# Performance work log

Measured on AMD Instinct MI355X. Metric: run time of the kernel, lower is better.

The kernel has to match this reference:

```python
import jax, jax.numpy as jnp
import numpy as np

# FreqEncoder constants (from init_kwargs)
X_DIM = 3
MIN_DEG = 0.0
MAX_DEG = 8.0
NUM_SCALES = 8            # max_deg - min_deg
RES = 128                 # 2 ** log2_res
NUM_CH = 8                # num_feats (channels per grid)
STD = 0.001
P = 262144                # number of sample points


def setup_inputs() -> dict:
    key = jax.random.key(0)
    k1, k2 = jax.random.split(key)
    x = jax.random.uniform(k1, (P, X_DIM), dtype=jnp.float32)
    # learned 1D grids: [num_scales*2*x_dim, num_channels, res]
    features = jax.random.normal(k2, (NUM_SCALES * 2 * X_DIM, NUM_CH, RES), dtype=jnp.float32) * STD
    return {"x": x, "features": features}


def reference(x, features):
    S, D, C, res = NUM_SCALES, X_DIM, NUM_CH, RES
    N = S * 2 * D  # number of 1D grids
    p = x.shape[0]

    # scales = 2 ** linspace(min_deg, max_deg, num_scales)  (matches torch.linspace)
    scales = 2.0 ** jnp.linspace(MIN_DEG, MAX_DEG, S).astype(x.dtype)  # [S]

    xb = x[:, None, :] * scales[None, :, None]                     # [P, S, D]
    latent = jnp.sin(jnp.stack([xb, xb + 0.5 * jnp.pi], axis=-2))  # [P, S, 2, D]

    # values in [-1, 1] used as grid_sample y-coords; one grid per (s, phase, d)
    v = latent.reshape(p, N).T                                     # [N, P]

    # align_corners=True bilinear unnormalization along the res axis
    pos = (v + 1.0) * 0.5 * (res - 1)                              # [N, P] in [0, res-1]
    i0f = jnp.floor(pos)
    frac = pos - i0f                                               # [N, P]
    i0 = jnp.clip(i0f, 0, res - 1).astype(jnp.int32)
    i1 = jnp.clip(i0 + 1, 0, res - 1)

    idx0 = jnp.broadcast_to(i0[:, None, :], (N, C, p))
    idx1 = jnp.broadcast_to(i1[:, None, :], (N, C, p))
    f0 = jnp.take_along_axis(features, idx0, axis=2)               # [N, C, P]
    f1 = jnp.take_along_axis(features, idx1, axis=2)               # [N, C, P]
    fs = f0 * (1.0 - frac[:, None, :]) + f1 * frac[:, None, :]     # [N, C, P]

    # [N, C, P] -> [S, 2, D, C, P] -> [P, C, S, 2, D], add residual, flatten
    fs = fs.reshape(S, 2, D, C, p).transpose(4, 3, 0, 1, 2)
    out = (fs + latent[:, None, :, :, :]).reshape(p, C * S * 2 * D)

    # use_identity=True: prepend raw coordinates
    return jnp.concatenate([x, out], axis=-1)                      # [P, 3 + 384]
```

## Files before the change

kernel.cpp:

```cpp
#include <hip/hip_runtime.h>
#include <hip/hip_bf16.h>
#include <stdint.h>


constexpr int P_PTS = 262144;
constexpr int S_SC  = 8;
constexpr int D_DIM = 3;
constexpr int C_CH  = 8;
constexpr int RES   = 128;
constexpr int N_GR  = S_SC * 2 * D_DIM;
constexpr int OW    = 3 + C_CH * N_GR;
constexpr int KPB   = 32;
constexpr int CHUNKS = 8;
constexpr int PPB   = KPB * CHUNKS;
constexpr int BLK   = 1024;

constexpr float ENC_SCALE = 256.0f;
constexpr float DEC_SCALE = 1.0f / 256.0f;
constexpr float INV_2PI   = 0.15915494309189535f;

constexpr int LDS_TABLE_B = N_GR * RES * 8;
constexpr int LDS_SOUT_B  = KPB * OW * 4;
constexpr int LDS_SX_B    = PPB * D_DIM * 4;
constexpr int LDS_TOTAL_B = LDS_TABLE_B + 2 * LDS_SOUT_B + LDS_SX_B;

typedef float f32x2 __attribute__((ext_vector_type(2)));

__device__ uint2 g_tap[N_GR * RES];

__global__ __launch_bounds__(256) void feat_pack_kernel(const float* __restrict__ f) {
    int t = blockIdx.x * 256 + threadIdx.x;
    if (t >= N_GR * RES) return;
    int n = t / RES, i = t % RES;

    uint32_t d0, d1;
    {
        float a = f[(n * C_CH + 0) * RES + i] * ENC_SCALE;
        float b = f[(n * C_CH + 1) * RES + i] * ENC_SCALE;
        float c = f[(n * C_CH + 2) * RES + i] * ENC_SCALE;
        float e = f[(n * C_CH + 3) * RES + i] * ENC_SCALE;
        int lo = __builtin_amdgcn_cvt_pk_fp8_f32(a, b, 0, false);
        d0 = (uint32_t)__builtin_amdgcn_cvt_pk_fp8_f32(c, e, lo, true);
    }
    {
        float a = f[(n * C_CH + 4) * RES + i] * ENC_SCALE;
        float b = f[(n * C_CH + 5) * RES + i] * ENC_SCALE;
        float c = f[(n * C_CH + 6) * RES + i] * ENC_SCALE;
        float e = f[(n * C_CH + 7) * RES + i] * ENC_SCALE;
        int lo = __builtin_amdgcn_cvt_pk_fp8_f32(a, b, 0, false);
        d1 = (uint32_t)__builtin_amdgcn_cvt_pk_fp8_f32(c, e, lo, true);
    }
    g_tap[t] = make_uint2(d0, d1);
}

__global__ __launch_bounds__(1024) void freq_encode_kernel(const float* __restrict__ x,
                                                           float* __restrict__ out) {
    extern __shared__ char smem[];
    uint2* ld_tap = reinterpret_cast<uint2*>(smem);
    float* s_out0 = reinterpret_cast<float*>(smem + LDS_TABLE_B);
    float* s_out1 = reinterpret_cast<float*>(smem + LDS_TABLE_B + LDS_SOUT_B);
    float* s_x    = reinterpret_cast<float*>(smem + LDS_TABLE_B + 2 * LDS_SOUT_B);

    const int tid   = threadIdx.x;
    const int pbase = blockIdx.x * PPB;

    for (int i = tid; i < N_GR * RES; i += BLK) ld_tap[i] = g_tap[i];
    for (int i = tid; i < PPB * D_DIM; i += BLK) s_x[i] = x[(size_t)pbase * D_DIM + i];
    __syncthreads();

    auto do_compute = [&](int p0l, float* sbuf) {
        if (tid < KPB * D_DIM) {
            sbuf[(tid / D_DIM) * OW + (tid % D_DIM)] = s_x[p0l * D_DIM + tid];
        }
        for (int u = tid; u < KPB * N_GR; u += BLK) {
            int pl = u / N_GR;
            int n  = u % N_GR;
            int s  = n / (2 * D_DIM);
            int r  = n % (2 * D_DIM);
            int ph = r / D_DIM;
            int d  = r % D_DIM;

            float xv    = s_x[(p0l + pl) * D_DIM + d];
            float scale = exp2f((float)s * (8.0f / 7.0f));
            float rv    = fmaf(xv * scale, INV_2PI, ph ? 0.25f : 0.0f);
            float lat   = __builtin_amdgcn_sinf(__builtin_amdgcn_fractf(rv));

            float pos  = (lat + 1.0f) * 63.5f;
            float i0f  = floorf(pos);
            float frac = pos - i0f;
            int   i0   = (int)i0f;
            i0 = max(0, min(i0, RES - 1));
            int   i1   = min(i0 + 1, RES - 1);

            uint2 t0 = ld_tap[n * RES + i0];
            uint2 t1 = ld_tap[n * RES + i1];

            f32x2 a01 = __builtin_amdgcn_cvt_pk_f32_fp8(t0.x, false);
            f32x2 a23 = __builtin_amdgcn_cvt_pk_f32_fp8(t0.x, true);
            f32x2 a45 = __builtin_amdgcn_cvt_pk_f32_fp8(t0.y, false);
            f32x2 a67 = __builtin_amdgcn_cvt_pk_f32_fp8(t0.y, true);
            f32x2 b01 = __builtin_amdgcn_cvt_pk_f32_fp8(t1.x, false);
            f32x2 b23 = __builtin_amdgcn_cvt_pk_f32_fp8(t1.x, true);
            f32x2 b45 = __builtin_amdgcn_cvt_pk_f32_fp8(t1.y, false);
            f32x2 b67 = __builtin_amdgcn_cvt_pk_f32_fp8(t1.y, true);

            float omd = (1.0f - frac) * DEC_SCALE;
            float frd = frac * DEC_SCALE;

            float* dst = &sbuf[pl * OW + 3 + n];
            dst[0 * N_GR] = fmaf(a01[0], omd, fmaf(b01[0], frd, lat));
            dst[1 * N_GR] = fmaf(a01[1], omd, fmaf(b01[1], frd, lat));
            dst[2 * N_GR] = fmaf(a23[0], omd, fmaf(b23[0], frd, lat));
            dst[3 * N_GR] = fmaf(a23[1], omd, fmaf(b23[1], frd, lat));
            dst[4 * N_GR] = fmaf(a45[0], omd, fmaf(b45[0], frd, lat));
            dst[5 * N_GR] = fmaf(a45[1], omd, fmaf(b45[1], frd, lat));
            dst[6 * N_GR] = fmaf(a67[0], omd, fmaf(b67[0], frd, lat));
            dst[7 * N_GR] = fmaf(a67[1], omd, fmaf(b67[1], frd, lat));
        }
    };

    auto do_store = [&](int p0l, const float* sbuf) {
        constexpr int NV = KPB * OW / 4;
        const float4* src = reinterpret_cast<const float4*>(sbuf);
        float4*       dst = reinterpret_cast<float4*>(out + ((size_t)pbase + p0l) * OW);
        for (int i = tid; i < NV; i += BLK) {
            dst[i] = src[i];
        }
    };

    do_compute(0, s_out0);
    __syncthreads();
    for (int ch = 1; ch < CHUNKS; ++ch) {
        float* cur  = (ch & 1) ? s_out1 : s_out0;
        float* prev = (ch & 1) ? s_out0 : s_out1;
        do_store((ch - 1) * KPB, prev);
        do_compute(ch * KPB, cur);
        __syncthreads();
    }
    do_store((CHUNKS - 1) * KPB, ((CHUNKS - 1) & 1) ? s_out1 : s_out0);
}

extern "C" void kernel_launch(void* const* d_in, const int* in_sizes, int n_in,
                              void* d_out, int out_size, void* d_ws, size_t ws_size,
                              hipStream_t stream) {
    const float* x    = (const float*)d_in[0];
    const float* feat = (const float*)d_in[1];
    float*       out  = (float*)d_out;

    int n_taps = N_GR * RES;
    feat_pack_kernel<<<(n_taps + 255) / 256, 256, 0, stream>>>(feat);

    freq_encode_kernel<<<P_PTS / PPB, BLK, LDS_TOTAL_B, stream>>>(x, out);
}
```

Baseline: 88.80 us.

## Replace double-buffered chunk pipeline with single buffer and nontemporal stores

Halves the points per chunk and doubles the chunk count, so each chunk's 768 work items fit in one pass of the 1024-thread block. The double-buffered compute/store overlap is replaced by a single staging buffer with two barriers per chunk. Output writes now use nontemporal stores. This cuts LDS use, which may allow more resident blocks, and tightens launch bounds, but it serialises compute and store within each block and adds barriers.

New measurement: 101.4 us. 1.14x slower.

```diff
diff --git a/kernel.cpp b/kernel.cpp
--- a/kernel.cpp
+++ b/kernel.cpp
@@ -10,8 +10,8 @@
 constexpr int RES   = 128;
 constexpr int N_GR  = S_SC * 2 * D_DIM;
 constexpr int OW    = 3 + C_CH * N_GR;
-constexpr int KPB   = 32;
-constexpr int CHUNKS = 8;
+constexpr int KPB   = 16;
+constexpr int CHUNKS = 16;
 constexpr int PPB   = KPB * CHUNKS;
 constexpr int BLK   = 1024;
 
@@ -22,9 +22,10 @@
 constexpr int LDS_TABLE_B = N_GR * RES * 8;
 constexpr int LDS_SOUT_B  = KPB * OW * 4;
 constexpr int LDS_SX_B    = PPB * D_DIM * 4;
-constexpr int LDS_TOTAL_B = LDS_TABLE_B + 2 * LDS_SOUT_B + LDS_SX_B;
+constexpr int LDS_TOTAL_B = LDS_TABLE_B + LDS_SOUT_B + LDS_SX_B;
 
 typedef float f32x2 __attribute__((ext_vector_type(2)));
+typedef float f32x4 __attribute__((ext_vector_type(4)));
 
 __device__ uint2 g_tap[N_GR * RES];
 
@@ -53,28 +54,30 @@
     g_tap[t] = make_uint2(d0, d1);
 }
 
-__global__ __launch_bounds__(1024) void freq_encode_kernel(const float* __restrict__ x,
-                                                           float* __restrict__ out) {
+__global__ __launch_bounds__(1024, 8) void freq_encode_kernel(const float* __restrict__ x,
+                                                              float* __restrict__ out) {
     extern __shared__ char smem[];
     uint2* ld_tap = reinterpret_cast<uint2*>(smem);
-    float* s_out0 = reinterpret_cast<float*>(smem + LDS_TABLE_B);
-    float* s_out1 = reinterpret_cast<float*>(smem + LDS_TABLE_B + LDS_SOUT_B);
-    float* s_x    = reinterpret_cast<float*>(smem + LDS_TABLE_B + 2 * LDS_SOUT_B);
+    float* s_out  = reinterpret_cast<float*>(smem + LDS_TABLE_B);
+    float* s_x    = reinterpret_cast<float*>(smem + LDS_TABLE_B + LDS_SOUT_B);
 
     const int tid   = threadIdx.x;
     const int pbase = blockIdx.x * PPB;
 
     for (int i = tid; i < N_GR * RES; i += BLK) ld_tap[i] = g_tap[i];
-    for (int i = tid; i < PPB * D_DIM; i += BLK) s_x[i] = x[(size_t)pbase * D_DIM + i];
+    if (tid < PPB * D_DIM) s_x[tid] = x[(size_t)pbase * D_DIM + tid];
     __syncthreads();
 
-    auto do_compute = [&](int p0l, float* sbuf) {
+    for (int ch = 0; ch < CHUNKS; ++ch) {
+        const int p0l = ch * KPB;
+
         if (tid < KPB * D_DIM) {
-            sbuf[(tid / D_DIM) * OW + (tid % D_DIM)] = s_x[p0l * D_DIM + tid];
+            s_out[(tid / D_DIM) * OW + (tid % D_DIM)] = s_x[p0l * D_DIM + tid];
         }
-        for (int u = tid; u < KPB * N_GR; u += BLK) {
-            int pl = u / N_GR;
-            int n  = u % N_GR;
+
+        if (tid < KPB * N_GR) {
+            int pl = tid / N_GR;
+            int n  = tid % N_GR;
             int s  = n / (2 * D_DIM);
             int r  = n % (2 * D_DIM);
             int ph = r / D_DIM;
@@ -107,7 +110,7 @@
             float omd = (1.0f - frac) * DEC_SCALE;
             float frd = frac * DEC_SCALE;
 
-            float* dst = &sbuf[pl * OW + 3 + n];
+            float* dst = &s_out[pl * OW + 3 + n];
             dst[0 * N_GR] = fmaf(a01[0], omd, fmaf(b01[0], frd, lat));
             dst[1 * N_GR] = fmaf(a01[1], omd, fmaf(b01[1], frd, lat));
             dst[2 * N_GR] = fmaf(a23[0], omd, fmaf(b23[0], frd, lat));
@@ -117,27 +120,16 @@
             dst[6 * N_GR] = fmaf(a67[0], omd, fmaf(b67[0], frd, lat));
             dst[7 * N_GR] = fmaf(a67[1], omd, fmaf(b67[1], frd, lat));
         }
-    };
+        __syncthreads();
 
-    auto do_store = [&](int p0l, const float* sbuf) {
         constexpr int NV = KPB * OW / 4;
-        const float4* src = reinterpret_cast<const float4*>(sbuf);
-        float4*       dst = reinterpret_cast<float4*>(out + ((size_t)pbase + p0l) * OW);
+        const f32x4* src = reinterpret_cast<const f32x4*>(s_out);
+        f32x4*       dst = reinterpret_cast<f32x4*>(out + ((size_t)pbase + p0l) * OW);
         for (int i = tid; i < NV; i += BLK) {
-            dst[i] = src[i];
+            __builtin_nontemporal_store(src[i], &dst[i]);
         }
-    };
-
-    do_compute(0, s_out0);
-    __syncthreads();
-    for (int ch = 1; ch < CHUNKS; ++ch) {
-        float* cur  = (ch & 1) ? s_out1 : s_out0;
-        float* prev = (ch & 1) ? s_out0 : s_out1;
-        do_store((ch - 1) * KPB, prev);
-        do_compute(ch * KPB, cur);
         __syncthreads();
     }
-    do_store((CHUNKS - 1) * KPB, ((CHUNKS - 1) & 1) ? s_out1 : s_out0);
 }
 
 extern "C" void kernel_launch(void* const* d_in, const int* in_sizes, int n_in,
```
